# Optimization experiments

Measured on AMD Instinct MI355X. Metric: run time of the kernel, lower is better.

## Reference

```python
import jax, jax.numpy as jnp
import numpy as np

DT = 0.01  # integrator time step (fixed, as passed to forward_sensitivity_online)


def _step(W, x, v, dt):
    # One integrator step: learned linear force x @ W.T plus fixed harmonic force_fn(x) = -x
    f = -x + x @ W.T                 # [N, D]
    v_new = v + dt * f
    x_new = x + dt * v_new
    return x_new, v_new


def setup_inputs() -> dict:
    key = jax.random.key(0)
    k1, k2, k3 = jax.random.split(key, 3)
    N, D = 128, 64
    return {
        "x0": jax.random.normal(k1, (N, D), dtype=jnp.float32),
        "v0": jax.random.normal(k2, (N, D), dtype=jnp.float32),
        "force_weight": jax.random.normal(k3, (D, D), dtype=jnp.float32) * 0.05,
        "n_steps": 16,
        "store_every": 4,
    }


def reference(x0, v0, force_weight, n_steps, store_every):
    """Online forward-mode sensitivity propagation.

    Propagates d(state)/d(theta) alongside the state: at each step, linearize the
    integrator step and push all P = D*D parameter tangent directions through the
    JVP (vmapped), exactly mirroring the torch vmap-over-n_params jvp loop.
    Returns (trajectory of x stored every `store_every`, final Jacobian of x_T
    w.r.t. force_weight, shaped [*x0.shape, *W.shape]).
    """
    W = force_weight
    D = W.shape[0]
    P = D * D
    # one-hot tangent directions for the flattened parameter (torch get_tangent_dict)
    basis = jnp.eye(P, dtype=W.dtype).reshape(P, D, D)      # [P, D, D]
    jx0 = jnp.zeros((P,) + x0.shape, dtype=x0.dtype)        # [P, N, D]
    jv0 = jnp.zeros((P,) + v0.shape, dtype=v0.dtype)

    def scan_step(carry, _):
        x, v, jx, jv = carry
        (x_new, v_new), lin = jax.linearize(
            lambda W_, x_, v_: _step(W_, x_, v_, DT), W, x, v
        )
        # push all P tangent directions through the linearized step in one batch
        jx_new, jv_new = jax.vmap(lin)(basis, jx, jv)       # [P, N, D] each
        return (x_new, v_new, jx_new, jv_new), x_new

    (xT, vT, jxT, jvT), xs = jax.lax.scan(
        scan_step, (x0, v0, jx0, jv0), None, length=n_steps
    )
    # stored trajectory: x0 followed by every store_every-th step (n_steps//store_every + 1 frames)
    traj = jnp.concatenate([x0[None], xs], axis=0)[::store_every]
    # final_jacs reshape: movedim(0, -1).reshape(*x0.shape, *p.shape)
    jac = jnp.moveaxis(jxT, 0, -1).reshape(*x0.shape, D, D)  # [N, D, D, D]
    return traj, jac
```

## Files before the change

kernel.cpp:

```cpp
#include <hip/hip_runtime.h>

#define DT 0.01f
constexpr int N = 128;
constexpr int D = 64;
constexpr int T = 16;

__global__ __launch_bounds__(64) void traj_u_kernel(
    const float* __restrict__ x0, const float* __restrict__ v0,
    const float* __restrict__ Wg, float* __restrict__ X,
    float* __restrict__ UT, float* __restrict__ traj) {
  const int j = threadIdx.x;
  float w[D];
#pragma unroll
  for (int k = 0; k < D; ++k) w[k] = Wg[j * D + k];

  const int b = blockIdx.x;
  if (b < N) {
    const int n = b;
    float x = x0[n * D + j];
    float v = v0[n * D + j];
    traj[n * D + j] = x;
    X[n * D + j] = x;
    for (int t = 1; t <= T; ++t) {
      float f0 = 0.f, f1 = 0.f, f2 = 0.f, f3 = 0.f;
#pragma unroll
      for (int k = 0; k < D; k += 4) {
        f0 += __shfl(x, k + 0) * w[k + 0];
        f1 += __shfl(x, k + 1) * w[k + 1];
        f2 += __shfl(x, k + 2) * w[k + 2];
        f3 += __shfl(x, k + 3) * w[k + 3];
      }
      float f = ((f0 + f1) + (f2 + f3)) - x;
      v += DT * f;
      x += DT * v;
      if (t < T) X[t * (N * D) + n * D + j] = x;
      if ((t & 3) == 0) traj[(t >> 2) * (N * D) + n * D + j] = x;
    }
  } else {
    const int a = b - N;
    float u  = (j == a) ? DT * DT : 0.0f;
    float wv = (j == a) ? DT : 0.0f;
    UT[j * D + a] = u;
    for (int m = 1; m < T; ++m) {
      float s0 = 0.f, s1 = 0.f, s2 = 0.f, s3 = 0.f;
#pragma unroll
      for (int k = 0; k < D; k += 4) {
        s0 += __shfl(u, k + 0) * w[k + 0];
        s1 += __shfl(u, k + 1) * w[k + 1];
        s2 += __shfl(u, k + 2) * w[k + 2];
        s3 += __shfl(u, k + 3) * w[k + 3];
      }
      float s = ((s0 + s1) + (s2 + s3)) - u;
      wv += DT * s;
      u  += DT * wv;
      UT[m * (D * D) + j * D + a] = u;
    }
  }
}

__global__ __launch_bounds__(256) void jac_kernel(
    const float* __restrict__ X, const float* __restrict__ UT,
    float* __restrict__ jac) {
  __shared__ float Ujs[T][D];
  __shared__ float Xns[T][D];
  const int tid = threadIdx.x;
  const int n = blockIdx.x >> 6;
  const int j = blockIdx.x & 63;

#pragma unroll
  for (int r = 0; r < 4; ++r) {
    int idx = tid + r * 256;
    int t = idx >> 6, c = idx & 63;
    Ujs[t][c] = UT[(T - 1 - t) * (D * D) + j * D + c];
    Xns[t][c] = X[t * (N * D) + n * D + c];
  }
  __syncthreads();

  const int w = tid >> 6;
  const int l = tid & 63;
  const int a0 = w * 16 + (l >> 4) * 4;
  const int b0 = (l & 15) * 4;

  float4 acc0 = make_float4(0.f, 0.f, 0.f, 0.f);
  float4 acc1 = acc0, acc2 = acc0, acc3 = acc0;
#pragma unroll
  for (int t = 0; t < T; ++t) {
    const float4 xv = *(const float4*)&Xns[t][b0];
    const float4 uv = *(const float4*)&Ujs[t][a0];
    acc0.x += uv.x * xv.x; acc0.y += uv.x * xv.y; acc0.z += uv.x * xv.z; acc0.w += uv.x * xv.w;
    acc1.x += uv.y * xv.x; acc1.y += uv.y * xv.y; acc1.z += uv.y * xv.z; acc1.w += uv.y * xv.w;
    acc2.x += uv.z * xv.x; acc2.y += uv.z * xv.y; acc2.z += uv.z * xv.z; acc2.w += uv.z * xv.w;
    acc3.x += uv.w * xv.x; acc3.y += uv.w * xv.y; acc3.z += uv.w * xv.z; acc3.w += uv.w * xv.w;
  }

  float* out = jac + (size_t)blockIdx.x * (D * D);
  const int base = a0 * 64 + b0;
  *(float4*)&out[base +   0] = acc0;
  *(float4*)&out[base +  64] = acc1;
  *(float4*)&out[base + 128] = acc2;
  *(float4*)&out[base + 192] = acc3;
}

extern "C" void kernel_launch(void* const* d_in, const int* in_sizes, int n_in,
                              void* d_out, int out_size, void* d_ws, size_t ws_size,
                              hipStream_t stream) {
  const float* x0 = (const float*)d_in[0];
  const float* v0 = (const float*)d_in[1];
  const float* W  = (const float*)d_in[2];

  float* traj = (float*)d_out;
  float* jac  = (float*)d_out + 5 * N * D;

  float* X  = (float*)d_ws;
  float* UT = X + T * N * D;

  traj_u_kernel<<<dim3(N + D), dim3(64), 0, stream>>>(x0, v0, W, X, UT, traj);
  jac_kernel<<<dim3(N * D), dim3(256), 0, stream>>>(X, UT, jac);
}
```

Measured before the change: 162.8 us.

## Batch four j-slices per jac block with vectorized loads and nontemporal stores

Each jac_kernel block now computes four output j-slices instead of one. It reuses the shared X tile across them and cuts the grid by four. Shared-memory fills use float4 loads, and output writes use nontemporal vector stores to avoid polluting the cache on the 128 MB streaming write. The trade-off is fewer blocks, which means less parallelism, and a serial jj loop per block.

Measured after the change: 175.7 us. 1.08x slower.

```diff
diff --git a/kernel.cpp b/kernel.cpp
--- a/kernel.cpp
+++ b/kernel.cpp
@@ -4,6 +4,9 @@
 constexpr int N = 128;
 constexpr int D = 64;
 constexpr int T = 16;
+constexpr int JB = 4;
+
+typedef float f32x4 __attribute__((ext_vector_type(4)));
 
 __global__ __launch_bounds__(64) void traj_u_kernel(
     const float* __restrict__ x0, const float* __restrict__ v0,
@@ -61,18 +64,23 @@
 __global__ __launch_bounds__(256) void jac_kernel(
     const float* __restrict__ X, const float* __restrict__ UT,
     float* __restrict__ jac) {
-  __shared__ float Ujs[T][D];
   __shared__ float Xns[T][D];
+  __shared__ float Ujs[JB][T][D];
   const int tid = threadIdx.x;
-  const int n = blockIdx.x >> 6;
-  const int j = blockIdx.x & 63;
+  const int n  = blockIdx.x >> 4;
+  const int j0 = (blockIdx.x & 15) * JB;
 
+  {
+    const int t = tid >> 4, c4 = tid & 15;
+    *(float4*)&Xns[t][c4 * 4] =
+        *(const float4*)&X[t * (N * D) + n * D + c4 * 4];
+  }
 #pragma unroll
   for (int r = 0; r < 4; ++r) {
-    int idx = tid + r * 256;
-    int t = idx >> 6, c = idx & 63;
-    Ujs[t][c] = UT[(T - 1 - t) * (D * D) + j * D + c];
-    Xns[t][c] = X[t * (N * D) + n * D + c];
+    const int u = tid + r * 256;
+    const int jj = u >> 8, t = (u >> 4) & 15, a4 = u & 15;
+    *(float4*)&Ujs[jj][t][a4 * 4] =
+        *(const float4*)&UT[(T - 1 - t) * (D * D) + (j0 + jj) * D + a4 * 4];
   }
   __syncthreads();
 
@@ -81,24 +89,25 @@
   const int a0 = w * 16 + (l >> 4) * 4;
   const int b0 = (l & 15) * 4;
 
-  float4 acc0 = make_float4(0.f, 0.f, 0.f, 0.f);
-  float4 acc1 = acc0, acc2 = acc0, acc3 = acc0;
+#pragma unroll 1
+  for (int jj = 0; jj < JB; ++jj) {
+    f32x4 acc0 = (f32x4)(0.f);
+    f32x4 acc1 = acc0, acc2 = acc0, acc3 = acc0;
 #pragma unroll
-  for (int t = 0; t < T; ++t) {
-    const float4 xv = *(const float4*)&Xns[t][b0];
-    const float4 uv = *(const float4*)&Ujs[t][a0];
-    acc0.x += uv.x * xv.x; acc0.y += uv.x * xv.y; acc0.z += uv.x * xv.z; acc0.w += uv.x * xv.w;
-    acc1.x += uv.y * xv.x; acc1.y += uv.y * xv.y; acc1.z += uv.y * xv.z; acc1.w += uv.y * xv.w;
-    acc2.x += uv.z * xv.x; acc2.y += uv.z * xv.y; acc2.z += uv.z * xv.z; acc2.w += uv.z * xv.w;
-    acc3.x += uv.w * xv.x; acc3.y += uv.w * xv.y; acc3.z += uv.w * xv.z; acc3.w += uv.w * xv.w;
+    for (int t = 0; t < T; ++t) {
+      const f32x4 xv = *(const f32x4*)&Xns[t][b0];
+      const f32x4 uv = *(const f32x4*)&Ujs[jj][t][a0];
+      acc0 += uv.x * xv;
+      acc1 += uv.y * xv;
+      acc2 += uv.z * xv;
+      acc3 += uv.w * xv;
+    }
+    float* out = jac + ((size_t)(n * D + j0 + jj)) * (D * D) + a0 * 64 + b0;
+    __builtin_nontemporal_store(acc0, (f32x4*)(out +   0));
+    __builtin_nontemporal_store(acc1, (f32x4*)(out +  64));
+    __builtin_nontemporal_store(acc2, (f32x4*)(out + 128));
+    __builtin_nontemporal_store(acc3, (f32x4*)(out + 192));
   }
-
-  float* out = jac + (size_t)blockIdx.x * (D * D);
-  const int base = a0 * 64 + b0;
-  *(float4*)&out[base +   0] = acc0;
-  *(float4*)&out[base +  64] = acc1;
-  *(float4*)&out[base + 128] = acc2;
-  *(float4*)&out[base + 192] = acc3;
 }
 
 extern "C" void kernel_launch(void* const* d_in, const int* in_sizes, int n_in,
@@ -115,5 +124,5 @@
   float* UT = X + T * N * D;
 
   traj_u_kernel<<<dim3(N + D), dim3(64), 0, stream>>>(x0, v0, W, X, UT, traj);
-  jac_kernel<<<dim3(N * D), dim3(256), 0, stream>>>(X, UT, jac);
+  jac_kernel<<<dim3(N * (D / JB)), dim3(256), 0, stream>>>(X, UT, jac);
 }
```
